# Optimization experiments

Measured on AMD Instinct MI355X. Metric: run time of the kernel, lower is better.

Reference implementation:

```python
import jax, jax.numpy as jnp
import numpy as np

EPS_NORM = 1e-12  # F.normalize default eps
EPS_LN = 1e-5     # nn.LayerNorm default eps


def _bilinear(feat, uv):
    """Bilinear interpolation at float pixel coords (the Interpolator).
    feat: (B, d, H, W); uv: (B, P, 2) with uv[...,0]=x, uv[...,1]=y in pixel units.
    Returns val (B, P, d) and in-bounds mask (B, P)."""
    B, d, H, W = feat.shape
    x, y = uv[..., 0], uv[..., 1]
    x0f, y0f = jnp.floor(x), jnp.floor(y)
    wx, wy = x - x0f, y - y0f
    x0, y0 = x0f.astype(jnp.int32), y0f.astype(jnp.int32)
    valid = ((x >= 0) & (x <= W - 1) & (y >= 0) & (y <= H - 1)).astype(feat.dtype)
    ff = feat.reshape(B, d, H * W)
    def gather(xi, yi):
        xi = jnp.clip(xi, 0, W - 1)
        yi = jnp.clip(yi, 0, H - 1)
        idx = (yi * W + xi)[:, None, :]  # (B,1,P)
        return jnp.take_along_axis(ff, idx, axis=2)  # (B,d,P)
    v00 = gather(x0, y0)
    v10 = gather(x0 + 1, y0)
    v01 = gather(x0, y0 + 1)
    v11 = gather(x0 + 1, y0 + 1)
    wx_, wy_ = wx[:, None, :], wy[:, None, :]
    val = (v00 * (1 - wx_) * (1 - wy_) + v10 * wx_ * (1 - wy_)
           + v01 * (1 - wx_) * wy_ + v11 * wx_ * wy_)
    return val.transpose(0, 2, 1), valid  # (B,P,d), (B,P)


def _ln(x, w, b):
    mu = x.mean(-1, keepdims=True)
    var = ((x - mu) ** 2).mean(-1, keepdims=True)
    return (x - mu) * jax.lax.rsqrt(var + EPS_LN) * w + b


def _l2norm(x, axis):
    n = jnp.sqrt(jnp.sum(x * x, axis=axis, keepdims=True))
    return x / jnp.maximum(n, EPS_NORM)


def setup_inputs() -> dict:
    B, N, D, H, W = 4, 6, 128, 128, 128
    ks = jax.random.split(jax.random.key(0), 6)
    return {
        "query": jax.random.normal(ks[0], (B, D, H, W), jnp.float32),
        "ref": jax.random.normal(ks[1], (B, N, D, H, W), jnp.float32),
        "homo_uv": jax.random.uniform(ks[2], (B, N, 2, H, W), jnp.float32),
        "ln1_w": jnp.ones((D,), jnp.float32),
        "ln1_b": jnp.zeros((D,), jnp.float32),
        "ln2_w": jnp.ones((D,), jnp.float32),
        "ln2_b": jnp.zeros((D,), jnp.float32),
        "w1": jax.random.normal(ks[3], (D, 2 * D), jnp.float32) * 0.02,
        "b1": jnp.zeros((2 * D,), jnp.float32),
        "w2": jax.random.normal(ks[4], (2 * D, D), jnp.float32) * 0.02,
        "b2": jnp.zeros((D,), jnp.float32),
    }


def reference(query, ref, homo_uv, ln1_w, ln1_b, ln2_w, ln2_b, w1, b1, w2, b2):
    b, n, d, H, W = ref.shape
    P = H * W
    # (b n 2 H W) -> ((b n), P, 2), scaled to pixel coords
    uv = homo_uv.transpose(0, 1, 3, 4, 2).reshape(b * n, P, 2)
    uv = uv * jnp.array([W, H], dtype=uv.dtype)
    val, mask = _bilinear(ref.reshape(b * n, d, H, W), uv)  # (bn,P,d),(bn,P)
    key = _l2norm(val, axis=2).reshape(b, n, P, d)
    q = _l2norm(query.reshape(b, d, P), axis=1)
    dot = jnp.einsum('bdp,bnpd->bnp', q, key) * mask.reshape(b, n, P)
    att = jax.nn.softmax(dot, axis=1)  # softmax over views n
    z = jnp.einsum('bnp,bnpd->bpd', att, val.reshape(b, n, P, d))
    z = query + z.transpose(0, 2, 1).reshape(b, d, H, W)
    zt = z.reshape(b, d, P).transpose(0, 2, 1)  # (b, P, d)
    zt = _ln(zt, ln1_w, ln1_b)
    h = jax.nn.gelu(zt @ w1 + b1, approximate=False)
    zt = zt + h @ w2 + b2
    zt = _ln(zt, ln2_w, ln2_b)
    return zt.transpose(0, 2, 1).reshape(b, d, H, W)
```

## Files before the change

kernel.cpp:

```cpp
#include <hip/hip_runtime.h>

typedef unsigned short u16;
typedef unsigned int u32;
#define DEV __device__ __forceinline__

typedef short s16x8 __attribute__((ext_vector_type(8)));
typedef float f32x4 __attribute__((ext_vector_type(4)));

DEV float bfl(u16 u) { union { u32 i; float f; } c; c.i = ((u32)u) << 16; return c.f; }
DEV float bflo(u32 u) { union { u32 i; float f; } c; c.i = u << 16; return c.f; }
DEV float bfhi(u32 u) { union { u32 i; float f; } c; c.i = u & 0xffff0000u; return c.f; }
DEV u16 f2b(float f) {
    union { float f; u32 u; } c; c.f = f;
    u32 u = c.u;
    return (u16)((u + 0x7fffu + ((u >> 16) & 1u)) >> 16);
}

template <typename T> DEV float ld1(const T* p, size_t i);
template <> DEV float ld1<u16>(const u16* p, size_t i) { return bfl(p[i]); }
template <> DEV float ld1<float>(const float* p, size_t i) { return p[i]; }

template <typename T> DEV void st1(T* p, size_t i, float v);
template <> DEV void st1<u16>(u16* p, size_t i, float v) { p[i] = f2b(v); }
template <> DEV void st1<float>(float* p, size_t i, float v) { p[i] = v; }

template <typename T> DEV T fromf(float f);
template <> DEV u16 fromf<u16>(float f) { return f2b(f); }
template <> DEV float fromf<float>(float f) { return f; }

DEV f32x4 mfma16(s16x8 a, s16x8 b, f32x4 c) {
    return __builtin_amdgcn_mfma_f32_16x16x32_bf16(a, b, c, 0, 0, 0);
}

static const int Bq = 4, Nv = 6, Pp = 128 * 128;

__global__ void kdetect(const void* ones, u32* flag) {
    if (threadIdx.x == 0 && blockIdx.x == 0)
        *flag = (*(const u32*)ones == 0x3F803F80u) ? 1u : 0u;
}

__global__ __launch_bounds__(256) void kprew(const void* w1, const void* w2, u16* wsw,
                                             const u32* __restrict__ flag) {
    int t = blockIdx.x * 256 + threadIdx.x;
    int isw2 = t >> 15;
    int i = t & 32767;
    int j = i & 7, lane = (i >> 3) & 63, tile = i >> 9;
    int g = lane >> 4, c = lane & 15;
    int k, col, src;
    if (!isw2) { int kt = tile >> 4, nt = tile & 15; k = kt * 32 + g * 8 + j; col = nt * 16 + c; src = k * 256 + col; }
    else       { int kt = tile >> 3, mt = tile & 7;  k = kt * 32 + g * 8 + j; col = mt * 16 + c; src = k * 128 + col; }
    const void* wsrc = isw2 ? w2 : w1;
    float wv = (*flag) ? bfl(((const u16*)wsrc)[src]) : ((const float*)wsrc)[src];
    u16 hi = f2b(wv);
    u16 lo = f2b(wv - bfl(hi));
    int base = isw2 ? 65536 : 0;
    wsw[base + i] = hi;
    wsw[base + 32768 + i] = lo;
}

template <typename TI, typename TO>
DEV void trans_body(const TI* src, TO* dst, long soff, long sstride, long dstride,
                    TO (*tile)[65]) {
    const int C = 16384, R = 128;
    const TI* s = src + soff + (size_t)blockIdx.z * sstride;
    TO* d = dst + (size_t)blockIdx.z * dstride;
    int p0 = blockIdx.x * 64, r0 = blockIdx.y * 64;
    int tc = threadIdx.x & 63, tr = threadIdx.x >> 6;
#pragma unroll
    for (int i = 0; i < 16; ++i) {
        int r = tr + i * 4;
        tile[r][tc] = fromf<TO>(ld1<TI>(s, (size_t)(r0 + r) * C + p0 + tc));
    }
    __syncthreads();
#pragma unroll
    for (int i = 0; i < 16; ++i) {
        int pr = tr + i * 4;
        d[(size_t)(p0 + pr) * R + r0 + tc] = tile[tc][pr];
    }
}

__global__ __launch_bounds__(256) void ktransB(const void* src, u16* dst, long soff,
                                               long sstride, long dstride,
                                               const u32* __restrict__ flag) {
    __shared__ __align__(16) u16 tile[64][65];
    if (*flag) trans_body<u16, u16>((const u16*)src, dst, soff, sstride, dstride, tile);
    else       trans_body<float, u16>((const float*)src, dst, soff, sstride, dstride, tile);
}

__global__ __launch_bounds__(256) void ktransQ(const void* src, float* dst,
                                               long sstride, long dstride,
                                               const u32* __restrict__ flag) {
    __shared__ __align__(16) float tile[64][65];
    if (*flag) trans_body<u16, float>((const u16*)src, dst, 0, sstride, dstride, tile);
    else       trans_body<float, float>((const float*)src, dst, 0, sstride, dstride, tile);
}

template <typename T>
DEV void attn4all_body(const u16* __restrict__ refT, const float* __restrict__ qT,
                       const T* __restrict__ huv, float* __restrict__ z) {
    int wid = (blockIdx.x * 256 + threadIdx.x) >> 6;
    int lane = threadIdx.x & 63;
    int sub = lane >> 4, ln16 = lane & 15, ch0 = ln16 * 8;
    int pg = wid * 4 + sub;
    int b = pg >> 14, p = pg & 16383;
    const T* huvb = huv + (size_t)b * Nv * 2 * Pp;
    const u16* refb = refT + (size_t)b * Nv * Pp * 128;

    const float* qp = qT + (size_t)pg * 128 + ch0;
    float4 qa = *(const float4*)qp;
    float4 qb = *(const float4*)(qp + 4);
    float q[8] = {qa.x, qa.y, qa.z, qa.w, qb.x, qb.y, qb.z, qb.w};

    float val[6][8], dt[6], v2[6], msk[6];
#pragma unroll
    for (int n = 0; n < 6; ++n) {
        float x = ld1<T>(huvb, (size_t)(n * 2 + 0) * Pp + p) * 128.f;
        float y = ld1<T>(huvb, (size_t)(n * 2 + 1) * Pp + p) * 128.f;
        float x0f = floorf(x), y0f = floorf(y);
        float wx = x - x0f, wy = y - y0f;
        int x0 = (int)x0f, y0 = (int)y0f;
        msk[n] = (x >= 0.f && x <= 127.f && y >= 0.f && y <= 127.f) ? 1.f : 0.f;
        int xa = min(max(x0, 0), 127), xb = min(max(x0 + 1, 0), 127);
        int ya = min(max(y0, 0), 127), yb = min(max(y0 + 1, 0), 127);
        const u16* ra = refb + ((size_t)n * Pp + (ya << 7)) * 128 + ch0;
        const u16* rb = refb + ((size_t)n * Pp + (yb << 7)) * 128 + ch0;
        uint4 u00 = *(const uint4*)(ra + (size_t)xa * 128);
        uint4 u10 = *(const uint4*)(ra + (size_t)xb * 128);
        uint4 u01 = *(const uint4*)(rb + (size_t)xa * 128);
        uint4 u11 = *(const uint4*)(rb + (size_t)xb * 128);
        float w00 = (1.f - wx) * (1.f - wy), w10 = wx * (1.f - wy);
        float w01 = (1.f - wx) * wy, w11 = wx * wy;
        const u32* a00 = (const u32*)&u00;
        const u32* a10 = (const u32*)&u10;
        const u32* a01 = (const u32*)&u01;
        const u32* a11 = (const u32*)&u11;
        float d_ = 0.f, s_ = 0.f;
#pragma unroll
        for (int c = 0; c < 4; ++c) {
            float lo = bflo(a00[c]) * w00 + bflo(a10[c]) * w10 + bflo(a01[c]) * w01 + bflo(a11[c]) * w11;
            float hi = bfhi(a00[c]) * w00 + bfhi(a10[c]) * w10 + bfhi(a01[c]) * w01 + bfhi(a11[c]) * w11;
            val[n][2 * c] = lo; val[n][2 * c + 1] = hi;
            d_ += q[2 * c] * lo + q[2 * c + 1] * hi;
            s_ += lo * lo + hi * hi;
        }
        dt[n] = d_; v2[n] = s_;
    }
    float qq = 0.f;
#pragma unroll
    for (int j = 0; j < 8; ++j) qq += q[j] * q[j];
#pragma unroll
    for (int off = 1; off < 16; off <<= 1) {
        qq += __shfl_xor(qq, off, 64);
#pragma unroll
        for (int n = 0; n < 6; ++n) {
            dt[n] += __shfl_xor(dt[n], off, 64);
            v2[n] += __shfl_xor(v2[n], off, 64);
        }
    }
    float qinv = 1.f / fmaxf(sqrtf(qq), 1e-12f);
    float dots[6], m = -1e30f;
#pragma unroll
    for (int n = 0; n < 6; ++n) {
        dots[n] = dt[n] * qinv / fmaxf(sqrtf(v2[n]), 1e-12f) * msk[n];
        m = fmaxf(m, dots[n]);
    }
    float es = 0.f, e[6];
#pragma unroll
    for (int n = 0; n < 6; ++n) { e[n] = __expf(dots[n] - m); es += e[n]; }
    float inv = 1.f / es;
#pragma unroll
    for (int n = 0; n < 6; ++n) e[n] *= inv;
    float zo[8];
#pragma unroll
    for (int j = 0; j < 8; ++j) {
        float zz = q[j];
#pragma unroll
        for (int n = 0; n < 6; ++n) zz += e[n] * val[n][j];
        zo[j] = zz;
    }
    float* zp = z + (size_t)pg * 128 + ch0;
    *(float4*)zp = make_float4(zo[0], zo[1], zo[2], zo[3]);
    *(float4*)(zp + 4) = make_float4(zo[4], zo[5], zo[6], zo[7]);
}

__global__ __launch_bounds__(256) void kattn4all(const u16* refT, const float* qT,
                                                 const void* huv, float* z,
                                                 const u32* __restrict__ flag) {
    if (*flag) attn4all_body<u16>(refT, qT, (const u16*)huv, z);
    else       attn4all_body<float>(refT, qT, (const float*)huv, z);
}

template <typename T>
DEV void attn4_body(const u16* __restrict__ refT, const T* __restrict__ qp,
                    const T* __restrict__ huv, float* __restrict__ z, int b) {
    int wid = (blockIdx.x * 256 + threadIdx.x) >> 6;
    int lane = threadIdx.x & 63;
    int sub = lane >> 4, ln16 = lane & 15, ch0 = ln16 * 8;
    int p = wid * 4 + sub;
    const T* huvb = huv + (size_t)b * Nv * 2 * Pp;

    float q[8];
#pragma unroll
    for (int j = 0; j < 8; ++j)
        q[j] = ld1<T>(qp, ((size_t)(b * 128 + ch0 + j)) * Pp + p);

    float val[6][8], dt[6], v2[6], msk[6];
#pragma unroll
    for (int n = 0; n < 6; ++n) {
        float x = ld1<T>(huvb, (size_t)(n * 2 + 0) * Pp + p) * 128.f;
        float y = ld1<T>(huvb, (size_t)(n * 2 + 1) * Pp + p) * 128.f;
        float x0f = floorf(x), y0f = floorf(y);
        float wx = x - x0f, wy = y - y0f;
        int x0 = (int)x0f, y0 = (int)y0f;
        msk[n] = (x >= 0.f && x <= 127.f && y >= 0.f && y <= 127.f) ? 1.f : 0.f;
        int xa = min(max(x0, 0), 127), xb = min(max(x0 + 1, 0), 127);
        int ya = min(max(y0, 0), 127), yb = min(max(y0 + 1, 0), 127);
        const u16* ra = refT + ((size_t)n * Pp + (ya << 7)) * 128 + ch0;
        const u16* rb = refT + ((size_t)n * Pp + (yb << 7)) * 128 + ch0;
        uint4 u00 = *(const uint4*)(ra + (size_t)xa * 128);
        uint4 u10 = *(const uint4*)(ra + (size_t)xb * 128);
        uint4 u01 = *(const uint4*)(rb + (size_t)xa * 128);
        uint4 u11 = *(const uint4*)(rb + (size_t)xb * 128);
        float w00 = (1.f - wx) * (1.f - wy), w10 = wx * (1.f - wy);
        float w01 = (1.f - wx) * wy, w11 = wx * wy;
        const u32* a00 = (const u32*)&u00;
        const u32* a10 = (const u32*)&u10;
        const u32* a01 = (const u32*)&u01;
        const u32* a11 = (const u32*)&u11;
        float d_ = 0.f, s_ = 0.f;
#pragma unroll
        for (int c = 0; c < 4; ++c) {
            float lo = bflo(a00[c]) * w00 + bflo(a10[c]) * w10 + bflo(a01[c]) * w01 + bflo(a11[c]) * w11;
            float hi = bfhi(a00[c]) * w00 + bfhi(a10[c]) * w10 + bfhi(a01[c]) * w01 + bfhi(a11[c]) * w11;
            val[n][2 * c] = lo; val[n][2 * c + 1] = hi;
            d_ += q[2 * c] * lo + q[2 * c + 1] * hi;
            s_ += lo * lo + hi * hi;
        }
        dt[n] = d_; v2[n] = s_;
    }
    float qq = 0.f;
#pragma unroll
    for (int j = 0; j < 8; ++j) qq += q[j] * q[j];
#pragma unroll
    for (int off = 1; off < 16; off <<= 1) {
        qq += __shfl_xor(qq, off, 64);
#pragma unroll
        for (int n = 0; n < 6; ++n) {
            dt[n] += __shfl_xor(dt[n], off, 64);
            v2[n] += __shfl_xor(v2[n], off, 64);
        }
    }
    float qinv = 1.f / fmaxf(sqrtf(qq), 1e-12f);
    float dots[6], m = -1e30f;
#pragma unroll
    for (int n = 0; n < 6; ++n) {
        dots[n] = dt[n] * qinv / fmaxf(sqrtf(v2[n]), 1e-12f) * msk[n];
        m = fmaxf(m, dots[n]);
    }
    float es = 0.f, e[6];
#pragma unroll
    for (int n = 0; n < 6; ++n) { e[n] = __expf(dots[n] - m); es += e[n]; }
    float inv = 1.f / es;
#pragma unroll
    for (int n = 0; n < 6; ++n) e[n] *= inv;
    float zo[8];
#pragma unroll
    for (int j = 0; j < 8; ++j) {
        float zz = q[j];
#pragma unroll
        for (int n = 0; n < 6; ++n) zz += e[n] * val[n][j];
        zo[j] = zz;
    }
    float* zp = z + ((size_t)b * Pp + p) * 128 + ch0;
    *(float4*)zp = make_float4(zo[0], zo[1], zo[2], zo[3]);
    *(float4*)(zp + 4) = make_float4(zo[4], zo[5], zo[6], zo[7]);
}

__global__ __launch_bounds__(256) void kattn4q(const u16* refT, const void* qp,
                                               const void* huv, float* z, int b,
                                               const u32* __restrict__ flag) {
    if (*flag) attn4_body<u16>(refT, (const u16*)qp, (const u16*)huv, z, b);
    else       attn4_body<float>(refT, (const float*)qp, (const float*)huv, z, b);
}

template <typename T>
DEV void attn_old_body(const T* refp, const T* qp, const T* huv, float* z, int b) {
    const int P_ = Pp;
    int gw = (blockIdx.x * 256 + threadIdx.x) >> 6;
    int lane = threadIdx.x & 63;
    int nw = (gridDim.x * 256) >> 6;
    int ch0 = lane * 2;
    const T* huvb = huv + (size_t)b * Nv * 2 * P_;

    for (int p = gw; p < P_; p += nw) {
        float q0 = ld1<T>(qp, ((size_t)(b * 128 + ch0)) * P_ + p);
        float q1 = ld1<T>(qp, ((size_t)(b * 128 + ch0 + 1)) * P_ + p);
        float va[6], vb[6], dt[6], v2[6], msk[6];
#pragma unroll
        for (int n = 0; n < 6; ++n) {
            float x = ld1<T>(huvb, (size_t)(n * 2 + 0) * P_ + p) * 128.f;
            float y = ld1<T>(huvb, (size_t)(n * 2 + 1) * P_ + p) * 128.f;
            float x0f = floorf(x), y0f = floorf(y);
            float wx = x - x0f, wy = y - y0f;
            int x0 = (int)x0f, y0 = (int)y0f;
            msk[n] = (x >= 0.f && x <= 127.f && y >= 0.f && y <= 127.f) ? 1.f : 0.f;
            int xa = min(max(x0, 0), 127), xb = min(max(x0 + 1, 0), 127);
            int ya = min(max(y0, 0), 127), yb = min(max(y0 + 1, 0), 127);
            const T* base = refp + (((size_t)(b * Nv + n) * 128 + ch0) * P_);
            int i00 = (ya << 7) + xa, i10 = (ya << 7) + xb;
            int i01 = (yb << 7) + xa, i11 = (yb << 7) + xb;
            float c00a = ld1<T>(base, i00), c00b = ld1<T>(base, (size_t)P_ + i00);
            float c10a = ld1<T>(base, i10), c10b = ld1<T>(base, (size_t)P_ + i10);
            float c01a = ld1<T>(base, i01), c01b = ld1<T>(base, (size_t)P_ + i01);
            float c11a = ld1<T>(base, i11), c11b = ld1<T>(base, (size_t)P_ + i11);
            float w00 = (1.f - wx) * (1.f - wy), w10 = wx * (1.f - wy);
            float w01 = (1.f - wx) * wy, w11 = wx * wy;
            float A = c00a * w00 + c10a * w10 + c01a * w01 + c11a * w11;
            float Bv = c00b * w00 + c10b * w10 + c01b * w01 + c11b * w11;
            va[n] = A; vb[n] = Bv;
            dt[n] = q0 * A + q1 * Bv;
            v2[n] = A * A + Bv * Bv;
        }
        float qq = q0 * q0 + q1 * q1;
#pragma unroll
        for (int off = 32; off; off >>= 1) {
            qq += __shfl_xor(qq, off, 64);
#pragma unroll
            for (int n = 0; n < 6; ++n) {
                dt[n] += __shfl_xor(dt[n], off, 64);
                v2[n] += __shfl_xor(v2[n], off, 64);
            }
        }
        float qinv = 1.f / fmaxf(sqrtf(qq), 1e-12f);
        float dots[6], m = -1e30f;
#pragma unroll
        for (int n = 0; n < 6; ++n) {
            dots[n] = dt[n] * qinv / fmaxf(sqrtf(v2[n]), 1e-12f) * msk[n];
            m = fmaxf(m, dots[n]);
        }
        float es = 0.f, e[6];
#pragma unroll
        for (int n = 0; n < 6; ++n) { e[n] = __expf(dots[n] - m); es += e[n]; }
        float inv = 1.f / es;
        float za = q0, zb = q1;
#pragma unroll
        for (int n = 0; n < 6; ++n) { float a = e[n] * inv; za += a * va[n]; zb += a * vb[n]; }
        float2 zz; zz.x = za; zz.y = zb;
        *(float2*)(z + ((size_t)b * P_ + p) * 128 + ch0) = zz;
    }
}

__global__ __launch_bounds__(256) void kattn_old(const void* refp, const void* qp,
                                                 const void* huv, float* z, int b,
                                                 const u32* __restrict__ flag) {
    if (*flag) attn_old_body<u16>((const u16*)refp, (const u16*)qp, (const u16*)huv, z, b);
    else       attn_old_body<float>((const float*)refp, (const float*)qp, (const float*)huv, z, b);
}

template <typename T, bool LO>
DEV void mlp_mfma_body(const float* z, const T* ln1w, const T* ln1b, const T* ln2w,
                       const T* ln2b, const u16* __restrict__ wsw, const T* b1g,
                       const T* b2g, T* outp, u16 (*ztT)[136], char* smem2) {
    u16* hB = (u16*)smem2;
    float(*o)[132] = (float(*)[132])smem2;

    int t = threadIdx.x, lane = t & 63, wv = t >> 6;
    int l15 = lane & 15, lg = lane >> 4;
    long r0 = (long)blockIdx.x * 64;

    for (int i = wv * 16; i < wv * 16 + 16; ++i) {
        float2 xv = *(const float2*)(z + (size_t)(r0 + i) * 128 + lane * 2);
        float s = xv.x + xv.y, s2 = xv.x * xv.x + xv.y * xv.y;
#pragma unroll
        for (int off = 32; off; off >>= 1) { s += __shfl_xor(s, off, 64); s2 += __shfl_xor(s2, off, 64); }
        float mu = s * 0.0078125f;
        float var = s2 * 0.0078125f - mu * mu;
        float rs = rsqrtf(var + 1e-5f);
        float a0 = (xv.x - mu) * rs * ld1<T>(ln1w, lane * 2) + ld1<T>(ln1b, lane * 2);
        float a1 = (xv.y - mu) * rs * ld1<T>(ln1w, lane * 2 + 1) + ld1<T>(ln1b, lane * 2 + 1);
        *(u32*)&ztT[i][lane * 2] = (u32)f2b(a0) | ((u32)f2b(a1) << 16);
    }
    __syncthreads();

    f32x4 acc[4][4];
#pragma unroll
    for (int a_ = 0; a_ < 4; ++a_)
#pragma unroll
        for (int b_ = 0; b_ < 4; ++b_) acc[a_][b_] = (f32x4){0.f, 0.f, 0.f, 0.f};

#pragma unroll
    for (int kt = 0; kt < 4; ++kt) {
        s16x8 af[4];
#pragma unroll
        for (int mt = 0; mt < 4; ++mt)
            af[mt] = *(const s16x8*)&ztT[mt * 16 + l15][kt * 32 + lg * 8];
#pragma unroll
        for (int ntl = 0; ntl < 4; ++ntl) {
            const u16* bp = wsw + ((size_t)((kt * 16 + wv * 4 + ntl) * 64 + lane)) * 8;
            s16x8 bh = *(const s16x8*)bp;
#pragma unroll
            for (int mt = 0; mt < 4; ++mt) acc[mt][ntl] = mfma16(af[mt], bh, acc[mt][ntl]);
            if (LO) {
                s16x8 bl = *(const s16x8*)(bp + 32768);
#pragma unroll
                for (int mt = 0; mt < 4; ++mt) acc[mt][ntl] = mfma16(af[mt], bl, acc[mt][ntl]);
            }
        }
    }

#pragma unroll
    for (int ntl = 0; ntl < 4; ++ntl) {
        int n = (wv * 4 + ntl) * 16 + l15;
        float bb = ld1<T>(b1g, n);
        u16* hp = hB + ((n >> 3) * 64) * 8 + (n & 7);
#pragma unroll
        for (int mt = 0; mt < 4; ++mt) {
            f32x4 v = acc[mt][ntl];
#pragma unroll
            for (int r = 0; r < 4; ++r) {
                float x = v[r] + bb;
                float g = 0.5f * x * (1.f + erff(x * 0.70710678118654752f));
                hp[(mt * 16 + lg * 4 + r) * 8] = f2b(g);
            }
        }
    }
    __syncthreads();

    f32x4 acc2[2][4];
#pragma unroll
    for (int a_ = 0; a_ < 2; ++a_)
#pragma unroll
        for (int b_ = 0; b_ < 4; ++b_) acc2[a_][b_] = (f32x4){0.f, 0.f, 0.f, 0.f};

#pragma unroll
    for (int kt = 0; kt < 8; ++kt) {
        s16x8 bfr[4];
#pragma unroll
        for (int p4 = 0; p4 < 4; ++p4)
            bfr[p4] = *(const s16x8*)&hB[((kt * 4 + lg) * 64 + p4 * 16 + l15) * 8];
#pragma unroll
        for (int mtl = 0; mtl < 2; ++mtl) {
            const u16* ap = wsw + 65536 + ((size_t)((kt * 8 + wv * 2 + mtl) * 64 + lane)) * 8;
            s16x8 ah = *(const s16x8*)ap;
#pragma unroll
            for (int p4 = 0; p4 < 4; ++p4) acc2[mtl][p4] = mfma16(ah, bfr[p4], acc2[mtl][p4]);
            if (LO) {
                s16x8 al = *(const s16x8*)(ap + 32768);
#pragma unroll
                for (int p4 = 0; p4 < 4; ++p4) acc2[mtl][p4] = mfma16(al, bfr[p4], acc2[mtl][p4]);
            }
        }
    }
    __syncthreads();

#pragma unroll
    for (int mtl = 0; mtl < 2; ++mtl) {
        int ch0 = (wv * 2 + mtl) * 16 + lg * 4;
        float b2v[4];
#pragma unroll
        for (int r = 0; r < 4; ++r) b2v[r] = ld1<T>(b2g, ch0 + r);
#pragma unroll
        for (int p4 = 0; p4 < 4; ++p4) {
            int pt = p4 * 16 + l15;
            const u16* rz = &ztT[pt][ch0];
            f32x4 v = acc2[mtl][p4];
            float4 ov;
            ov.x = v[0] + b2v[0] + bfl(rz[0]);
            ov.y = v[1] + b2v[1] + bfl(rz[1]);
            ov.z = v[2] + b2v[2] + bfl(rz[2]);
            ov.w = v[3] + b2v[3] + bfl(rz[3]);
            *(float4*)&o[pt][ch0] = ov;
        }
    }
    __syncthreads();

    for (int i = wv * 16; i < wv * 16 + 16; ++i) {
        float2 xv = *(const float2*)&o[i][lane * 2];
        float s = xv.x + xv.y, s2 = xv.x * xv.x + xv.y * xv.y;
#pragma unroll
        for (int off = 32; off; off >>= 1) { s += __shfl_xor(s, off, 64); s2 += __shfl_xor(s2, off, 64); }
        float mu = s * 0.0078125f;
        float var = s2 * 0.0078125f - mu * mu;
        float rs = rsqrtf(var + 1e-5f);
        o[i][lane * 2] = (xv.x - mu) * rs * ld1<T>(ln2w, lane * 2) + ld1<T>(ln2b, lane * 2);
        o[i][lane * 2 + 1] = (xv.y - mu) * rs * ld1<T>(ln2w, lane * 2 + 1) + ld1<T>(ln2b, lane * 2 + 1);
    }
    __syncthreads();

    long bb = r0 >> 14;
    int p0 = (int)(r0 & 16383);
    for (int ch = wv; ch < 128; ch += 4)
        st1<T>(outp, (size_t)((bb * 128 + ch) << 14) + p0 + lane, o[lane][ch]);
}

__global__ __launch_bounds__(256) void kmlp_mfma(const float* z, const void* ln1w,
                                                 const void* ln1b, const void* ln2w,
                                                 const void* ln2b, const u16* wsw,
                                                 const void* b1g, const void* b2g,
                                                 void* outp, const u32* __restrict__ flag) {
    __shared__ __align__(16) u16 ztT[64][136];
    __shared__ __align__(16) char smem2[33792];
    if (*flag)
        mlp_mfma_body<u16, false>(z, (const u16*)ln1w, (const u16*)ln1b, (const u16*)ln2w,
                                  (const u16*)ln2b, wsw, (const u16*)b1g, (const u16*)b2g,
                                  (u16*)outp, ztT, smem2);
    else
        mlp_mfma_body<float, true>(z, (const float*)ln1w, (const float*)ln1b, (const float*)ln2w,
                                   (const float*)ln2b, wsw, (const float*)b1g, (const float*)b2g,
                                   (float*)outp, ztT, smem2);
}

template <typename T>
DEV void mlp_body(const float* z,
                  const T* ln1w, const T* ln1b, const T* ln2w, const T* ln2b,
                  const T* w1g, const T* b1g, const T* w2g, const T* b2g, T* outp,
                  u16 (*ztT)[72], char* smem2) {
    u16(*hT)[72] = (u16(*)[72])smem2;
    float(*o)[130] = (float(*)[130])smem2;

    int t = threadIdx.x, lane = t & 63, wv = t >> 6;
    long r0 = (long)blockIdx.x * 64;

    for (int i = wv * 16; i < wv * 16 + 16; ++i) {
        float2 xv = *(const float2*)(z + (size_t)(r0 + i) * 128 + lane * 2);
        float s = xv.x + xv.y, s2 = xv.x * xv.x + xv.y * xv.y;
#pragma unroll
        for (int off = 32; off; off >>= 1) { s += __shfl_xor(s, off, 64); s2 += __shfl_xor(s2, off, 64); }
        float mu = s * 0.0078125f;
        float var = s2 * 0.0078125f - mu * mu;
        float rs = rsqrtf(var + 1e-5f);
        float a0 = (xv.x - mu) * rs * ld1<T>(ln1w, lane * 2) + ld1<T>(ln1b, lane * 2);
        float a1 = (xv.y - mu) * rs * ld1<T>(ln1w, lane * 2 + 1) + ld1<T>(ln1b, lane * 2 + 1);
        ztT[lane * 2][i] = f2b(a0);
        ztT[lane * 2 + 1][i] = f2b(a1);
    }
    __syncthreads();

    {
        float acc[64];
#pragma unroll
        for (int i = 0; i < 64; ++i) acc[i] = 0.f;
        for (int k = 0; k < 128; ++k) {
            float wv1 = ld1<T>(w1g, (size_t)k * 256 + t);
#pragma unroll
            for (int q8 = 0; q8 < 8; ++q8) {
                uint4 zv = *(const uint4*)&ztT[k][q8 * 8];
                acc[q8 * 8 + 0] += bflo(zv.x) * wv1; acc[q8 * 8 + 1] += bfhi(zv.x) * wv1;
                acc[q8 * 8 + 2] += bflo(zv.y) * wv1; acc[q8 * 8 + 3] += bfhi(zv.y) * wv1;
                acc[q8 * 8 + 4] += bflo(zv.z) * wv1; acc[q8 * 8 + 5] += bfhi(zv.z) * wv1;
                acc[q8 * 8 + 6] += bflo(zv.w) * wv1; acc[q8 * 8 + 7] += bfhi(zv.w) * wv1;
            }
        }
        float bb = ld1<T>(b1g, t);
#pragma unroll
        for (int q8 = 0; q8 < 8; ++q8) {
            u32 pk[4];
#pragma unroll
            for (int pp = 0; pp < 4; ++pp) {
                float x0v = acc[q8 * 8 + pp * 2] + bb;
                float x1v = acc[q8 * 8 + pp * 2 + 1] + bb;
                float g0 = 0.5f * x0v * (1.f + erff(x0v * 0.70710678118654752f));
                float g1 = 0.5f * x1v * (1.f + erff(x1v * 0.70710678118654752f));
                pk[pp] = (u32)f2b(g0) | ((u32)f2b(g1) << 16);
            }
            *(uint4*)&hT[t][q8 * 8] = make_uint4(pk[0], pk[1], pk[2], pk[3]);
        }
    }
    __syncthreads();

    int j2 = t & 127, hh = t >> 7;
    float acc2[32];
#pragma unroll
    for (int i = 0; i < 32; ++i) acc2[i] = 0.f;
    for (int k = 0; k < 256; ++k) {
        float wv2 = ld1<T>(w2g, (size_t)k * 128 + j2);
#pragma unroll
        for (int q8 = 0; q8 < 4; ++q8) {
            uint4 hv = *(const uint4*)&hT[k][hh * 32 + q8 * 8];
            acc2[q8 * 8 + 0] += bflo(hv.x) * wv2; acc2[q8 * 8 + 1] += bfhi(hv.x) * wv2;
            acc2[q8 * 8 + 2] += bflo(hv.y) * wv2; acc2[q8 * 8 + 3] += bfhi(hv.y) * wv2;
            acc2[q8 * 8 + 4] += bflo(hv.z) * wv2; acc2[q8 * 8 + 5] += bfhi(hv.z) * wv2;
            acc2[q8 * 8 + 6] += bflo(hv.w) * wv2; acc2[q8 * 8 + 7] += bfhi(hv.w) * wv2;
        }
    }
    __syncthreads();

    {
        float bb2 = ld1<T>(b2g, j2);
#pragma unroll
        for (int q8 = 0; q8 < 4; ++q8) {
            uint4 rz = *(const uint4*)&ztT[j2][hh * 32 + q8 * 8];
            o[hh * 32 + q8 * 8 + 0][j2] = acc2[q8 * 8 + 0] + bb2 + bflo(rz.x);
            o[hh * 32 + q8 * 8 + 1][j2] = acc2[q8 * 8 + 1] + bb2 + bfhi(rz.x);
            o[hh * 32 + q8 * 8 + 2][j2] = acc2[q8 * 8 + 2] + bb2 + bflo(rz.y);
            o[hh * 32 + q8 * 8 + 3][j2] = acc2[q8 * 8 + 3] + bb2 + bfhi(rz.y);
            o[hh * 32 + q8 * 8 + 4][j2] = acc2[q8 * 8 + 4] + bb2 + bflo(rz.z);
            o[hh * 32 + q8 * 8 + 5][j2] = acc2[q8 * 8 + 5] + bb2 + bfhi(rz.z);
            o[hh * 32 + q8 * 8 + 6][j2] = acc2[q8 * 8 + 6] + bb2 + bflo(rz.w);
            o[hh * 32 + q8 * 8 + 7][j2] = acc2[q8 * 8 + 7] + bb2 + bfhi(rz.w);
        }
    }
    __syncthreads();

    for (int i = wv * 16; i < wv * 16 + 16; ++i) {
        float2 xv = *(const float2*)&o[i][lane * 2];
        float s = xv.x + xv.y, s2 = xv.x * xv.x + xv.y * xv.y;
#pragma unroll
        for (int off = 32; off; off >>= 1) { s += __shfl_xor(s, off, 64); s2 += __shfl_xor(s2, off, 64); }
        float mu = s * 0.0078125f;
        float var = s2 * 0.0078125f - mu * mu;
        float rs = rsqrtf(var + 1e-5f);
        o[i][lane * 2] = (xv.x - mu) * rs * ld1<T>(ln2w, lane * 2) + ld1<T>(ln2b, lane * 2);
        o[i][lane * 2 + 1] = (xv.y - mu) * rs * ld1<T>(ln2w, lane * 2 + 1) + ld1<T>(ln2b, lane * 2 + 1);
    }
    __syncthreads();

    long bb = r0 >> 14;
    int p0 = (int)(r0 & 16383);
    for (int ch = wv; ch < 128; ch += 4)
        st1<T>(outp, (size_t)((bb * 128 + ch) << 14) + p0 + lane, o[lane][ch]);
}

__global__ __launch_bounds__(256) void kmlp(const float* z,
                                            const void* ln1w, const void* ln1b,
                                            const void* ln2w, const void* ln2b,
                                            const void* w1g, const void* b1g,
                                            const void* w2g, const void* b2g,
                                            void* outp, const u32* __restrict__ flag) {
    __shared__ __align__(16) u16 ztT[128][72];
    __shared__ __align__(16) char smem2[36864];
    if (*flag)
        mlp_body<u16>(z, (const u16*)ln1w, (const u16*)ln1b, (const u16*)ln2w, (const u16*)ln2b,
                      (const u16*)w1g, (const u16*)b1g, (const u16*)w2g, (const u16*)b2g,
                      (u16*)outp, ztT, smem2);
    else
        mlp_body<float>(z, (const float*)ln1w, (const float*)ln1b, (const float*)ln2w, (const float*)ln2b,
                        (const float*)w1g, (const float*)b1g, (const float*)w2g, (const float*)b2g,
                        (float*)outp, ztT, smem2);
}

extern "C" void kernel_launch(void* const* d_in, const int* in_sizes, int n_in,
                              void* d_out, int out_size, void* d_ws, size_t ws_size,
                              hipStream_t stream) {
    const void* query = d_in[0];
    const void* ref = d_in[1];
    const void* huv = d_in[2];
    const void* ln1w = d_in[3];
    const void* ln1b = d_in[4];
    const void* ln2w = d_in[5];
    const void* ln2b = d_in[6];
    const void* w1 = d_in[7];
    const void* b1 = d_in[8];
    const void* w2 = d_in[9];
    const void* b2 = d_in[10];
    char* ws = (char*)d_ws;

    const long CHW = (long)128 * Pp;
    const size_t ZF = (size_t)Bq * Pp * 128 * 4;
    const size_t REFT = (size_t)Nv * Pp * 128 * 2;
    const size_t QTSZ = (size_t)Bq * Pp * 128 * 4;
    const size_t WSW = 262144;

    u32* flag = (u32*)ws;
    char* base = ws + 256;
    float* zbuf = (float*)base;

    size_t need2 = 256 + ZF + (size_t)Bq * REFT + QTSZ + WSW;
    if (ws_size >= need2) {
        u16* refTall = (u16*)(base + ZF);
        float* qT = (float*)(base + ZF + (size_t)Bq * REFT);
        u16* wsw = (u16*)(base + ZF + (size_t)Bq * REFT + QTSZ);

        kdetect<<<1, 64, 0, stream>>>(ln1w, flag);
        kprew<<<256, 256, 0, stream>>>(w1, w2, wsw, flag);
        ktransB<<<dim3(256, 2, 24), 256, 0, stream>>>(ref, refTall, 0, CHW, CHW, flag);
        ktransQ<<<dim3(256, 2, 4), 256, 0, stream>>>(query, qT, CHW, CHW, flag);
        kattn4all<<<4096, 256, 0, stream>>>(refTall, qT, huv, zbuf, flag);
        kmlp_mfma<<<1024, 256, 0, stream>>>(zbuf, ln1w, ln1b, ln2w, ln2b, wsw, b1, b2, d_out, flag);
        return;
    }

    u16* refT = (u16*)(base + ZF);
    int full = (ws_size >= 256 + ZF + REFT) ? 1 : 0;
    size_t woff = full ? (256 + ZF + REFT) : (256 + ZF);
    int use_mfma = (ws_size >= woff + WSW) ? 1 : 0;
    u16* wsw = (u16*)(ws + woff);

    kdetect<<<1, 64, 0, stream>>>(ln1w, flag);
    if (use_mfma) kprew<<<256, 256, 0, stream>>>(w1, w2, wsw, flag);

    if (full) {
        for (int b = 0; b < Bq; ++b) {
            ktransB<<<dim3(256, 2, 6), 256, 0, stream>>>(ref, refT, (long)b * Nv * CHW, CHW, CHW, flag);
            kattn4q<<<1024, 256, 0, stream>>>(refT, query, huv, zbuf, b, flag);
        }
    } else {
        for (int b = 0; b < Bq; ++b)
            kattn_old<<<1024, 256, 0, stream>>>(ref, query, huv, zbuf, b, flag);
    }

    if (use_mfma)
        kmlp_mfma<<<1024, 256, 0, stream>>>(zbuf, ln1w, ln1b, ln2w, ln2b, wsw, b1, b2, d_out, flag);
    else
        kmlp<<<1024, 256, 0, stream>>>(zbuf, ln1w, ln1b, ln2w, ln2b, w1, b1, w2, b2, d_out, flag);
}
```

Measured before the change: 464.1 us.

## Fuse attention gather with LN1/MLP/LN2 and merge ref/query transposes

Merges the two transpose kernels into a single staging launch, and fuses the bilinear attention kernel into the MLP kernel so each 64-pixel block computes z, applies LayerNorm1 and writes the bf16 tile straight into shared memory. This removes the fp32 z round-trip through global memory and one or two kernel launches. In exchange, the fused kernel has higher register and shared-memory pressure and runs with fewer blocks (1024 instead of 4096 for the attention phase), which may reduce latency hiding on the gathers.

```diff
diff --git a/kernel.cpp b/kernel.cpp
--- a/kernel.cpp
+++ b/kernel.cpp
@@ -60,10 +60,10 @@
 
 template <typename TI, typename TO>
 DEV void trans_body(const TI* src, TO* dst, long soff, long sstride, long dstride,
-                    TO (*tile)[65]) {
+                    TO (*tile)[65], int zi) {
     const int C = 16384, R = 128;
-    const TI* s = src + soff + (size_t)blockIdx.z * sstride;
-    TO* d = dst + (size_t)blockIdx.z * dstride;
+    const TI* s = src + soff + (size_t)zi * sstride;
+    TO* d = dst + (size_t)zi * dstride;
     int p0 = blockIdx.x * 64, r0 = blockIdx.y * 64;
     int tc = threadIdx.x & 63, tr = threadIdx.x >> 6;
 #pragma unroll
@@ -76,6 +76,22 @@
     for (int i = 0; i < 16; ++i) {
         int pr = tr + i * 4;
         d[(size_t)(p0 + pr) * R + r0 + tc] = tile[tc][pr];
+    }
+}
+
+__global__ __launch_bounds__(256) void kstage(const void* ref, const void* query,
+                                              u16* refT, float* qT,
+                                              const u32* __restrict__ flag) {
+    __shared__ __align__(16) float tilef[64][65];
+    const long CHW = (long)128 * Pp;
+    int zi = blockIdx.z;
+    if (zi < 24) {
+        u16(*tile)[65] = (u16(*)[65])tilef;
+        if (*flag) trans_body<u16, u16>((const u16*)ref, refT, 0, CHW, CHW, tile, zi);
+        else       trans_body<float, u16>((const float*)ref, refT, 0, CHW, CHW, tile, zi);
+    } else {
+        if (*flag) trans_body<u16, float>((const u16*)query, qT, 0, CHW, CHW, tilef, zi - 24);
+        else       trans_body<float, float>((const float*)query, qT, 0, CHW, CHW, tilef, zi - 24);
     }
 }
 
@@ -83,111 +99,252 @@
                                                long sstride, long dstride,
                                                const u32* __restrict__ flag) {
     __shared__ __align__(16) u16 tile[64][65];
-    if (*flag) trans_body<u16, u16>((const u16*)src, dst, soff, sstride, dstride, tile);
-    else       trans_body<float, u16>((const float*)src, dst, soff, sstride, dstride, tile);
-}
-
-__global__ __launch_bounds__(256) void ktransQ(const void* src, float* dst,
-                                               long sstride, long dstride,
-                                               const u32* __restrict__ flag) {
-    __shared__ __align__(16) float tile[64][65];
-    if (*flag) trans_body<u16, float>((const u16*)src, dst, 0, sstride, dstride, tile);
-    else       trans_body<float, float>((const float*)src, dst, 0, sstride, dstride, tile);
-}
-
-template <typename T>
-DEV void attn4all_body(const u16* __restrict__ refT, const float* __restrict__ qT,
-                       const T* __restrict__ huv, float* __restrict__ z) {
-    int wid = (blockIdx.x * 256 + threadIdx.x) >> 6;
-    int lane = threadIdx.x & 63;
-    int sub = lane >> 4, ln16 = lane & 15, ch0 = ln16 * 8;
-    int pg = wid * 4 + sub;
-    int b = pg >> 14, p = pg & 16383;
+    if (*flag) trans_body<u16, u16>((const u16*)src, dst, soff, sstride, dstride, tile, blockIdx.z);
+    else       trans_body<float, u16>((const float*)src, dst, soff, sstride, dstride, tile, blockIdx.z);
+}
+
+template <typename T, bool LO>
+DEV void fuse_body(const u16* __restrict__ refT, const float* __restrict__ qT,
+                   const T* __restrict__ huv,
+                   const T* ln1w, const T* ln1b, const T* ln2w, const T* ln2b,
+                   const u16* __restrict__ wsw, const T* b1g, const T* b2g, T* outp,
+                   u16 (*ztT)[136], char* smem2) {
+    u16* hB = (u16*)smem2;
+    float(*o)[132] = (float(*)[132])smem2;
+
+    int t = threadIdx.x, lane = t & 63, wv = t >> 6;
+    int l15 = lane & 15, lg = lane >> 4;
+    int ch0 = l15 * 8;
+    long r0 = (long)blockIdx.x * 64;
+    int b = (int)(r0 >> 14);
     const T* huvb = huv + (size_t)b * Nv * 2 * Pp;
-    const u16* refb = refT + (size_t)b * Nv * Pp * 128;
-
-    const float* qp = qT + (size_t)pg * 128 + ch0;
-    float4 qa = *(const float4*)qp;
-    float4 qb = *(const float4*)(qp + 4);
-    float q[8] = {qa.x, qa.y, qa.z, qa.w, qb.x, qb.y, qb.z, qb.w};
-
-    float val[6][8], dt[6], v2[6], msk[6];
-#pragma unroll
-    for (int n = 0; n < 6; ++n) {
-        float x = ld1<T>(huvb, (size_t)(n * 2 + 0) * Pp + p) * 128.f;
-        float y = ld1<T>(huvb, (size_t)(n * 2 + 1) * Pp + p) * 128.f;
-        float x0f = floorf(x), y0f = floorf(y);
-        float wx = x - x0f, wy = y - y0f;
-        int x0 = (int)x0f, y0 = (int)y0f;
-        msk[n] = (x >= 0.f && x <= 127.f && y >= 0.f && y <= 127.f) ? 1.f : 0.f;
-        int xa = min(max(x0, 0), 127), xb = min(max(x0 + 1, 0), 127);
-        int ya = min(max(y0, 0), 127), yb = min(max(y0 + 1, 0), 127);
-        const u16* ra = refb + ((size_t)n * Pp + (ya << 7)) * 128 + ch0;
-        const u16* rb = refb + ((size_t)n * Pp + (yb << 7)) * 128 + ch0;
-        uint4 u00 = *(const uint4*)(ra + (size_t)xa * 128);
-        uint4 u10 = *(const uint4*)(ra + (size_t)xb * 128);
-        uint4 u01 = *(const uint4*)(rb + (size_t)xa * 128);
-        uint4 u11 = *(const uint4*)(rb + (size_t)xb * 128);
-        float w00 = (1.f - wx) * (1.f - wy), w10 = wx * (1.f - wy);
-        float w01 = (1.f - wx) * wy, w11 = wx * wy;
-        const u32* a00 = (const u32*)&u00;
-        const u32* a10 = (const u32*)&u10;
-        const u32* a01 = (const u32*)&u01;
-        const u32* a11 = (const u32*)&u11;
-        float d_ = 0.f, s_ = 0.f;
+    const u16* refb = refT + (size_t)b * (size_t)Nv * Pp * 128;
+
+    float lw[8], lbv[8];
+#pragma unroll
+    for (int j = 0; j < 8; ++j) { lw[j] = ld1<T>(ln1w, ch0 + j); lbv[j] = ld1<T>(ln1b, ch0 + j); }
+
+    for (int it = 0; it < 4; ++it) {
+        int ptl = it * 16 + wv * 4 + lg;
+        size_t pg = (size_t)r0 + ptl;
+        int p = (int)(pg & 16383);
+
+        const float* qp = qT + pg * 128 + ch0;
+        float4 qa = *(const float4*)qp;
+        float4 qb = *(const float4*)(qp + 4);
+        float q[8] = {qa.x, qa.y, qa.z, qa.w, qb.x, qb.y, qb.z, qb.w};
+
+        float val[6][8], dt[6], v2[6], msk[6];
+#pragma unroll
+        for (int n = 0; n < 6; ++n) {
+            float x = ld1<T>(huvb, (size_t)(n * 2 + 0) * Pp + p) * 128.f;
+            float y = ld1<T>(huvb, (size_t)(n * 2 + 1) * Pp + p) * 128.f;
+            float x0f = floorf(x), y0f = floorf(y);
+            float wx = x - x0f, wy = y - y0f;
+            int x0 = (int)x0f, y0 = (int)y0f;
+            msk[n] = (x >= 0.f && x <= 127.f && y >= 0.f && y <= 127.f) ? 1.f : 0.f;
+            int xa = min(max(x0, 0), 127), xb = min(max(x0 + 1, 0), 127);
+            int ya = min(max(y0, 0), 127), yb = min(max(y0 + 1, 0), 127);
+            const u16* ra = refb + ((size_t)n * Pp + (ya << 7)) * 128 + ch0;
+            const u16* rb = refb + ((size_t)n * Pp + (yb << 7)) * 128 + ch0;
+            uint4 u00 = *(const uint4*)(ra + (size_t)xa * 128);
+            uint4 u10 = *(const uint4*)(ra + (size_t)xb * 128);
+            uint4 u01 = *(const uint4*)(rb + (size_t)xa * 128);
+            uint4 u11 = *(const uint4*)(rb + (size_t)xb * 128);
+            float w00 = (1.f - wx) * (1.f - wy), w10 = wx * (1.f - wy);
+            float w01 = (1.f - wx) * wy, w11 = wx * wy;
+            const u32* a00 = (const u32*)&u00;
+            const u32* a10 = (const u32*)&u10;
+            const u32* a01 = (const u32*)&u01;
+            const u32* a11 = (const u32*)&u11;
+            float d_ = 0.f, s_ = 0.f;
+#pragma unroll
+            for (int c = 0; c < 4; ++c) {
+                float lo = bflo(a00[c]) * w00 + bflo(a10[c]) * w10 + bflo(a01[c]) * w01 + bflo(a11[c]) * w11;
+                float hi = bfhi(a00[c]) * w00 + bfhi(a10[c]) * w10 + bfhi(a01[c]) * w01 + bfhi(a11[c]) * w11;
+                val[n][2 * c] = lo; val[n][2 * c + 1] = hi;
+                d_ += q[2 * c] * lo + q[2 * c + 1] * hi;
+                s_ += lo * lo + hi * hi;
+            }
+            dt[n] = d_; v2[n] = s_;
+        }
+        float qq = 0.f;
+#pragma unroll
+        for (int j = 0; j < 8; ++j) qq += q[j] * q[j];
+#pragma unroll
+        for (int off = 1; off < 16; off <<= 1) {
+            qq += __shfl_xor(qq, off, 64);
+#pragma unroll
+            for (int n = 0; n < 6; ++n) {
+                dt[n] += __shfl_xor(dt[n], off, 64);
+                v2[n] += __shfl_xor(v2[n], off, 64);
+            }
+        }
+        float qinv = 1.f / fmaxf(sqrtf(qq), 1e-12f);
+        float dots[6], m = -1e30f;
+#pragma unroll
+        for (int n = 0; n < 6; ++n) {
+            dots[n] = dt[n] * qinv / fmaxf(sqrtf(v2[n]), 1e-12f) * msk[n];
+            m = fmaxf(m, dots[n]);
+        }
+        float es = 0.f, e[6];
+#pragma unroll
+        for (int n = 0; n < 6; ++n) { e[n] = __expf(dots[n] - m); es += e[n]; }
+        float inv = 1.f / es;
+#pragma unroll
+        for (int n = 0; n < 6; ++n) e[n] *= inv;
+        float zo[8];
+#pragma unroll
+        for (int j = 0; j < 8; ++j) {
+            float zz = q[j];
+#pragma unroll
+            for (int n = 0; n < 6; ++n) zz += e[n] * val[n][j];
+            zo[j] = zz;
+        }
+        float s = 0.f, s2 = 0.f;
+#pragma unroll
+        for (int j = 0; j < 8; ++j) { s += zo[j]; s2 += zo[j] * zo[j]; }
+#pragma unroll
+        for (int off = 1; off < 16; off <<= 1) { s += __shfl_xor(s, off, 64); s2 += __shfl_xor(s2, off, 64); }
+        float mu = s * 0.0078125f;
+        float var = s2 * 0.0078125f - mu * mu;
+        float rs = rsqrtf(var + 1e-5f);
 #pragma unroll
         for (int c = 0; c < 4; ++c) {
-            float lo = bflo(a00[c]) * w00 + bflo(a10[c]) * w10 + bflo(a01[c]) * w01 + bflo(a11[c]) * w11;
-            float hi = bfhi(a00[c]) * w00 + bfhi(a10[c]) * w10 + bfhi(a01[c]) * w01 + bfhi(a11[c]) * w11;
-            val[n][2 * c] = lo; val[n][2 * c + 1] = hi;
-            d_ += q[2 * c] * lo + q[2 * c + 1] * hi;
-            s_ += lo * lo + hi * hi;
-        }
-        dt[n] = d_; v2[n] = s_;
-    }
-    float qq = 0.f;
-#pragma unroll
-    for (int j = 0; j < 8; ++j) qq += q[j] * q[j];
-#pragma unroll
-    for (int off = 1; off < 16; off <<= 1) {
-        qq += __shfl_xor(qq, off, 64);
-#pragma unroll
-        for (int n = 0; n < 6; ++n) {
-            dt[n] += __shfl_xor(dt[n], off, 64);
-            v2[n] += __shfl_xor(v2[n], off, 64);
-        }
-    }
-    float qinv = 1.f / fmaxf(sqrtf(qq), 1e-12f);
-    float dots[6], m = -1e30f;
-#pragma unroll
-    for (int n = 0; n < 6; ++n) {
-        dots[n] = dt[n] * qinv / fmaxf(sqrtf(v2[n]), 1e-12f) * msk[n];
-        m = fmaxf(m, dots[n]);
-    }
-    float es = 0.f, e[6];
-#pragma unroll
-    for (int n = 0; n < 6; ++n) { e[n] = __expf(dots[n] - m); es += e[n]; }
-    float inv = 1.f / es;
-#pragma unroll
-    for (int n = 0; n < 6; ++n) e[n] *= inv;
-    float zo[8];
-#pragma unroll
-    for (int j = 0; j < 8; ++j) {
-        float zz = q[j];
-#pragma unroll
-        for (int n = 0; n < 6; ++n) zz += e[n] * val[n][j];
-        zo[j] = zz;
-    }
-    float* zp = z + (size_t)pg * 128 + ch0;
-    *(float4*)zp = make_float4(zo[0], zo[1], zo[2], zo[3]);
-    *(float4*)(zp + 4) = make_float4(zo[4], zo[5], zo[6], zo[7]);
-}
-
-__global__ __launch_bounds__(256) void kattn4all(const u16* refT, const float* qT,
-                                                 const void* huv, float* z,
-                                                 const u32* __restrict__ flag) {
-    if (*flag) attn4all_body<u16>(refT, qT, (const u16*)huv, z);
-    else       attn4all_body<float>(refT, qT, (const float*)huv, z);
+            float a0 = (zo[2 * c] - mu) * rs * lw[2 * c] + lbv[2 * c];
+            float a1 = (zo[2 * c + 1] - mu) * rs * lw[2 * c + 1] + lbv[2 * c + 1];
+            *(u32*)&ztT[ptl][ch0 + 2 * c] = (u32)f2b(a0) | ((u32)f2b(a1) << 16);
+        }
+    }
+    __syncthreads();
+
+    f32x4 acc[4][4];
+#pragma unroll
+    for (int a_ = 0; a_ < 4; ++a_)
+#pragma unroll
+        for (int b_ = 0; b_ < 4; ++b_) acc[a_][b_] = (f32x4){0.f, 0.f, 0.f, 0.f};
+
+#pragma unroll
+    for (int kt = 0; kt < 4; ++kt) {
+        s16x8 af[4];
+#pragma unroll
+        for (int mt = 0; mt < 4; ++mt)
+            af[mt] = *(const s16x8*)&ztT[mt * 16 + l15][kt * 32 + lg * 8];
+#pragma unroll
+        for (int ntl = 0; ntl < 4; ++ntl) {
+            const u16* bp = wsw + ((size_t)((kt * 16 + wv * 4 + ntl) * 64 + lane)) * 8;
+            s16x8 bh = *(const s16x8*)bp;
+#pragma unroll
+            for (int mt = 0; mt < 4; ++mt) acc[mt][ntl] = mfma16(af[mt], bh, acc[mt][ntl]);
+            if (LO) {
+                s16x8 bl = *(const s16x8*)(bp + 32768);
+#pragma unroll
+                for (int mt = 0; mt < 4; ++mt) acc[mt][ntl] = mfma16(af[mt], bl, acc[mt][ntl]);
+            }
+        }
+    }
+
+#pragma unroll
+    for (int ntl = 0; ntl < 4; ++ntl) {
+        int n = (wv * 4 + ntl) * 16 + l15;
+        float bb = ld1<T>(b1g, n);
+        u16* hp = hB + ((n >> 3) * 64) * 8 + (n & 7);
+#pragma unroll
+        for (int mt = 0; mt < 4; ++mt) {
+            f32x4 v = acc[mt][ntl];
+#pragma unroll
+            for (int r = 0; r < 4; ++r) {
+                float x = v[r] + bb;
+                float g = 0.5f * x * (1.f + erff(x * 0.70710678118654752f));
+                hp[(mt * 16 + lg * 4 + r) * 8] = f2b(g);
+            }
+        }
+    }
+    __syncthreads();
+
+    f32x4 acc2[2][4];
+#pragma unroll
+    for (int a_ = 0; a_ < 2; ++a_)
+#pragma unroll
+        for (int b_ = 0; b_ < 4; ++b_) acc2[a_][b_] = (f32x4){0.f, 0.f, 0.f, 0.f};
+
+#pragma unroll
+    for (int kt = 0; kt < 8; ++kt) {
+        s16x8 bfr[4];
+#pragma unroll
+        for (int p4 = 0; p4 < 4; ++p4)
+            bfr[p4] = *(const s16x8*)&hB[((kt * 4 + lg) * 64 + p4 * 16 + l15) * 8];
+#pragma unroll
+        for (int mtl = 0; mtl < 2; ++mtl) {
+            const u16* ap = wsw + 65536 + ((size_t)((kt * 8 + wv * 2 + mtl) * 64 + lane)) * 8;
+            s16x8 ah = *(const s16x8*)ap;
+#pragma unroll
+            for (int p4 = 0; p4 < 4; ++p4) acc2[mtl][p4] = mfma16(ah, bfr[p4], acc2[mtl][p4]);
+            if (LO) {
+                s16x8 al = *(const s16x8*)(ap + 32768);
+#pragma unroll
+                for (int p4 = 0; p4 < 4; ++p4) acc2[mtl][p4] = mfma16(al, bfr[p4], acc2[mtl][p4]);
+            }
+        }
+    }
+    __syncthreads();
+
+#pragma unroll
+    for (int mtl = 0; mtl < 2; ++mtl) {
+        int c0 = (wv * 2 + mtl) * 16 + lg * 4;
+        float b2v[4];
+#pragma unroll
+        for (int r = 0; r < 4; ++r) b2v[r] = ld1<T>(b2g, c0 + r);
+#pragma unroll
+        for (int p4 = 0; p4 < 4; ++p4) {
+            int pt = p4 * 16 + l15;
+            const u16* rz = &ztT[pt][c0];
+            f32x4 v = acc2[mtl][p4];
+            float4 ov;
+            ov.x = v[0] + b2v[0] + bfl(rz[0]);
+            ov.y = v[1] + b2v[1] + bfl(rz[1]);
+            ov.z = v[2] + b2v[2] + bfl(rz[2]);
+            ov.w = v[3] + b2v[3] + bfl(rz[3]);
+            *(float4*)&o[pt][c0] = ov;
+        }
+    }
+    __syncthreads();
+
+    for (int i = wv * 16; i < wv * 16 + 16; ++i) {
+        float2 xv = *(const float2*)&o[i][lane * 2];
+        float s = xv.x + xv.y, s2 = xv.x * xv.x + xv.y * xv.y;
+#pragma unroll
+        for (int off = 32; off; off >>= 1) { s += __shfl_xor(s, off, 64); s2 += __shfl_xor(s2, off, 64); }
+        float mu = s * 0.0078125f;
+        float var = s2 * 0.0078125f - mu * mu;
+        float rs = rsqrtf(var + 1e-5f);
+        o[i][lane * 2] = (xv.x - mu) * rs * ld1<T>(ln2w, lane * 2) + ld1<T>(ln2b, lane * 2);
+        o[i][lane * 2 + 1] = (xv.y - mu) * rs * ld1<T>(ln2w, lane * 2 + 1) + ld1<T>(ln2b, lane * 2 + 1);
+    }
+    __syncthreads();
+
+    long bb = r0 >> 14;
+    int p0 = (int)(r0 & 16383);
+    for (int ch = wv; ch < 128; ch += 4)
+        st1<T>(outp, (size_t)((bb * 128 + ch) << 14) + p0 + lane, o[lane][ch]);
+}
+
+__global__ __launch_bounds__(256) void kfuse(const u16* refT, const float* qT,
+                                             const void* huv, const void* ln1w,
+                                             const void* ln1b, const void* ln2w,
+                                             const void* ln2b, const u16* wsw,
+                                             const void* b1g, const void* b2g,
+                                             void* outp, const u32* __restrict__ flag) {
+    __shared__ __align__(16) u16 ztT[64][136];
+    __shared__ __align__(16) char smem2[33792];
+    if (*flag)
+        fuse_body<u16, false>(refT, qT, (const u16*)huv, (const u16*)ln1w, (const u16*)ln1b,
+                              (const u16*)ln2w, (const u16*)ln2b, wsw, (const u16*)b1g,
+                              (const u16*)b2g, (u16*)outp, ztT, smem2);
+    else
+        fuse_body<float, true>(refT, qT, (const float*)huv, (const float*)ln1w, (const float*)ln1b,
+                               (const float*)ln2w, (const float*)ln2b, wsw, (const float*)b1g,
+                               (const float*)b2g, (float*)outp, ztT, smem2);
 }
 
 template <typename T>
@@ -455,21 +612,21 @@
 
 #pragma unroll
     for (int mtl = 0; mtl < 2; ++mtl) {
-        int ch0 = (wv * 2 + mtl) * 16 + lg * 4;
+        int c0 = (wv * 2 + mtl) * 16 + lg * 4;
         float b2v[4];
 #pragma unroll
-        for (int r = 0; r < 4; ++r) b2v[r] = ld1<T>(b2g, ch0 + r);
+        for (int r = 0; r < 4; ++r) b2v[r] = ld1<T>(b2g, c0 + r);
 #pragma unroll
         for (int p4 = 0; p4 < 4; ++p4) {
             int pt = p4 * 16 + l15;
-            const u16* rz = &ztT[pt][ch0];
+            const u16* rz = &ztT[pt][c0];
             f32x4 v = acc2[mtl][p4];
             float4 ov;
             ov.x = v[0] + b2v[0] + bfl(rz[0]);
             ov.y = v[1] + b2v[1] + bfl(rz[1]);
             ov.z = v[2] + b2v[2] + bfl(rz[2]);
             ov.w = v[3] + b2v[3] + bfl(rz[3]);
-            *(float4*)&o[pt][ch0] = ov;
+            *(float4*)&o[pt][c0] = ov;
         }
     }
     __syncthreads();
@@ -663,23 +820,22 @@
 
     u32* flag = (u32*)ws;
     char* base = ws + 256;
-    float* zbuf = (float*)base;
-
-    size_t need2 = 256 + ZF + (size_t)Bq * REFT + QTSZ + WSW;
+
+    size_t need2 = 256 + (size_t)Bq * REFT + QTSZ + WSW;
     if (ws_size >= need2) {
-        u16* refTall = (u16*)(base + ZF);
-        float* qT = (float*)(base + ZF + (size_t)Bq * REFT);
-        u16* wsw = (u16*)(base + ZF + (size_t)Bq * REFT + QTSZ);
+        u16* refTall = (u16*)base;
+        float* qT = (float*)(base + (size_t)Bq * REFT);
+        u16* wsw = (u16*)(base + (size_t)Bq * REFT + QTSZ);
 
         kdetect<<<1, 64, 0, stream>>>(ln1w, flag);
         kprew<<<256, 256, 0, stream>>>(w1, w2, wsw, flag);
-        ktransB<<<dim3(256, 2, 24), 256, 0, stream>>>(ref, refTall, 0, CHW, CHW, flag);
-        ktransQ<<<dim3(256, 2, 4), 256, 0, stream>>>(query, qT, CHW, CHW, flag);
-        kattn4all<<<4096, 256, 0, stream>>>(refTall, qT, huv, zbuf, flag);
-        kmlp_mfma<<<1024, 256, 0, stream>>>(zbuf, ln1w, ln1b, ln2w, ln2b, wsw, b1, b2, d_out, flag);
+        kstage<<<dim3(256, 2, 28), 256, 0, stream>>>(ref, query, refTall, qT, flag);
+        kfuse<<<1024, 256, 0, stream>>>(refTall, qT, huv, ln1w, ln1b, ln2w, ln2b,
+                                        wsw, b1, b2, d_out, flag);
         return;
     }
 
+    float* zbuf = (float*)base;
     u16* refT = (u16*)(base + ZF);
     int full = (ws_size >= 256 + ZF + REFT) ? 1 : 0;
     size_t woff = full ? (256 + ZF + REFT) : (256 + ZF);
```

Measured after the change: 486.9 us. 4.9% more time.
